# Performance work log

Measured on AMD Instinct MI355X. Metric: run time of the kernel, lower is better.

## Reference

```python
import jax, jax.numpy as jnp
import numpy as np

B, S, D = 2, 1024, 7168
H, HD, RD, QL = 64, 128, 64, 1536
EPS = 1e-6
SOFTMAX_SCALE = HD ** (-0.5)


def _rope_interleave(x, cos, sin):
    """Interleaved RoPE (pairs x[2i], x[2i+1]); x: [T, n, RD], cos/sin: [T, RD]."""
    x1 = x[..., 0::2]
    x2 = x[..., 1::2]
    c = cos[:, None, 0::2]
    s = sin[:, None, 0::2]
    o1 = x1 * c - x2 * s
    o2 = x2 * c + x1 * s
    return jnp.stack([o1, o2], axis=-1).reshape(x.shape)


def setup_inputs() -> dict:
    key = jax.random.key(0)
    ks = jax.random.split(key, 8)
    x = jax.random.normal(ks[0], (B, S, D), dtype=jnp.float32) * 0.02
    qr = jax.random.normal(ks[1], (B * S, QL), dtype=jnp.float32) * 0.02
    # real interleaved-RoPE cos/sin tables, tiled over batch
    pos = jnp.arange(S, dtype=jnp.float32)
    inv_freq = 1.0 / (10000.0 ** (jnp.arange(0, RD, 2, dtype=jnp.float32) / RD))
    freqs = pos[:, None] * inv_freq[None, :]                      # [S, RD/2]
    cos = jnp.repeat(jnp.cos(freqs), 2, axis=-1)                  # [S, RD]
    sin = jnp.repeat(jnp.sin(freqs), 2, axis=-1)
    cos = jnp.tile(cos, (B, 1))                                   # [B*S, RD]
    sin = jnp.tile(sin, (B, 1))
    wq_b_w = jax.random.normal(ks[2], (QL, H * HD), dtype=jnp.float32) * (QL ** -0.5)
    wk_w = jax.random.normal(ks[3], (D, HD), dtype=jnp.float32) * (D ** -0.5)
    wproj_w = jax.random.normal(ks[4], (D, H), dtype=jnp.float32) * (D ** -0.5)
    ln_gamma = jnp.ones((HD,), dtype=jnp.float32)
    ln_beta = jnp.ones((HD,), dtype=jnp.float32)  # module inits bias to ones
    return {"x": x, "qr": qr, "cos": cos, "sin": sin, "wq_b_w": wq_b_w,
            "wk_w": wk_w, "wproj_w": wproj_w, "ln_gamma": ln_gamma, "ln_beta": ln_beta}


def reference(x, qr, cos, sin, wq_b_w, wk_w, wproj_w, ln_gamma, ln_beta):
    b, s, d = x.shape
    t = b * s
    xf = x.reshape(t, d)
    # ---- query path: low-rank up-proj, split rope/nope, interleaved RoPE ----
    q = (qr @ wq_b_w).reshape(t, H, HD)
    q_pe, q_nope = q[..., :RD], q[..., RD:]
    q_pe = _rope_interleave(q_pe, cos, sin)
    q = jnp.concatenate([q_pe, q_nope], axis=-1).reshape(b, s, H, HD)
    # ---- per-head gating weights ----
    w = (xf @ wproj_w).reshape(b, s, H)
    # ---- key path: project, LayerNorm, RoPE on rope slice ----
    kp = xf @ wk_w                                                # [T, HD]
    mu = jnp.mean(kp, axis=-1, keepdims=True)
    var = jnp.mean(jnp.square(kp - mu), axis=-1, keepdims=True)
    kn = (kp - mu) * jax.lax.rsqrt(var + EPS) * ln_gamma + ln_beta
    k_pe, k_nope = kn[..., :RD], kn[..., RD:]
    k_pe = _rope_interleave(k_pe[:, None, :], cos, sin)[:, 0]
    k = jnp.concatenate([k_pe, k_nope], axis=-1).reshape(b, s, HD)
    # ---- lightning-indexer scores: weighted ReLU(q.k) summed over heads ----
    logits = jnp.einsum("bqhd,bkd->bqhk", q, k)                   # [B,S,H,S]
    scores = SOFTMAX_SCALE * jnp.einsum("bqh,bqhk->bqk", w, jax.nn.relu(logits))
    return scores
```

## Files before the change

### kernel.cpp

```cpp
#include <hip/hip_runtime.h>

typedef unsigned short u16;
typedef unsigned int   u32;

typedef __bf16 bf16x8 __attribute__((ext_vector_type(8)));
typedef float  f32x4  __attribute__((ext_vector_type(4)));

__device__ __forceinline__ float bf2f(u16 u){ u32 x = ((u32)u) << 16; return __builtin_bit_cast(float, x); }
__device__ __forceinline__ u16 f2bf(float f){
  u32 u = __builtin_bit_cast(u32, f);
  u32 r = (u + 0x7FFFu + ((u >> 16) & 1u)) >> 16;
  return (u16)r;
}
__device__ __forceinline__ u32 pk2bf(float a, float b){
  u32 ua = __builtin_bit_cast(u32, a) + 0x8000u;
  u32 ub = __builtin_bit_cast(u32, b) + 0x8000u;
  return __builtin_amdgcn_perm(ub, ua, 0x07060302u);
}
__device__ __forceinline__ void glds16(const void* g, void* l){
  __builtin_amdgcn_global_load_lds((const __attribute__((address_space(1))) void*)g,
                                   (__attribute__((address_space(3))) void*)l, 16, 0, 0);
}

__global__ __launch_bounds__(256) void transpose_f32_bf16(const float* __restrict__ src,
                                                          u16* __restrict__ dst, int R, int C){
  __shared__ u16 tile[32][33];
  int c0 = blockIdx.x * 32, r0 = blockIdx.y * 32;
  int tx = threadIdx.x & 31, ty = threadIdx.x >> 5;
  #pragma unroll
  for (int i = ty; i < 32; i += 8) tile[i][tx] = f2bf(src[(size_t)(r0 + i) * C + (c0 + tx)]);
  __syncthreads();
  #pragma unroll
  for (int i = ty; i < 32; i += 8) dst[(size_t)(c0 + i) * R + (r0 + tx)] = tile[tx][i];
}

__global__ __launch_bounds__(256) void cvt_f32_bf16(const float* __restrict__ src,
                                                    u16* __restrict__ dst){
  size_t i = ((size_t)blockIdx.x * 256 + threadIdx.x) * 8;
  const float4* a4 = (const float4*)(src + i);
  float4 f0 = a4[0], f1 = a4[1];
  u32 w[4] = { pk2bf(f0.x, f0.y), pk2bf(f0.z, f0.w), pk2bf(f1.x, f1.y), pk2bf(f1.z, f1.w) };
  *(uint4*)(dst + i) = *(const uint4*)w;
}

__global__ __launch_bounds__(256) void proj_splitk(const float* __restrict__ X,
    const u16* __restrict__ BT, float* __restrict__ P){
  constexpr int Kf = 7168;
  const int s = blockIdx.x, m0 = blockIdx.y * 64;
  const int kbase = s * 448;
  __shared__ u16 As[2 * 64 * 36];
  __shared__ u16 Bs[2 * 192 * 32];
  const int tid = threadIdx.x, wave = tid >> 6, lane = tid & 63;
  const int row = lane & 15, quad = lane >> 4;
  const int wm = (wave & 1) * 32, wn = (wave >> 1) * 96;

  const f32x4 zero = {0.f, 0.f, 0.f, 0.f};
  f32x4 acc[2][6];
  #pragma unroll
  for (int mt = 0; mt < 2; ++mt)
    #pragma unroll
    for (int nt = 0; nt < 6; ++nt) acc[mt][nt] = zero;

  for (int kb = 0; kb < 7; ++kb) {
    int k0 = kbase + kb * 64;
    #pragma unroll
    for (int c = 0; c < 6; ++c) {
      int chunk = wave * 6 + c;
      int kc = chunk / 12, rem = chunk % 12;
      int r = rem * 16 + (lane >> 2), col = (lane & 3) * 8;
      glds16(BT + (size_t)r * Kf + k0 + kc * 32 + col, (void*)&Bs[chunk * 512]);
    }
    #pragma unroll
    for (int c = 0; c < 2; ++c) {
      int idx = tid + c * 256;
      int r = idx >> 3, kf = (idx & 7) * 8;
      const float4* ap = (const float4*)(X + (size_t)(m0 + r) * Kf + k0 + kf);
      float4 f0 = ap[0], f1 = ap[1];
      u32 w[4] = { pk2bf(f0.x, f0.y), pk2bf(f0.z, f0.w), pk2bf(f1.x, f1.y), pk2bf(f1.z, f1.w) };
      *(uint4*)&As[(kf >> 5) * 2304 + r * 36 + (kf & 31)] = *(const uint4*)w;
    }
    __syncthreads();
    #pragma unroll
    for (int ks = 0; ks < 2; ++ks) {
      bf16x8 af[2], bfr[6];
      #pragma unroll
      for (int mt = 0; mt < 2; ++mt) af[mt] = *(const bf16x8*)&As[ks * 2304 + (wm + mt * 16 + row) * 36 + quad * 8];
      #pragma unroll
      for (int nt = 0; nt < 6; ++nt) bfr[nt] = *(const bf16x8*)&Bs[ks * 6144 + (wn + nt * 16 + row) * 32 + quad * 8];
      #pragma unroll
      for (int mt = 0; mt < 2; ++mt)
        #pragma unroll
        for (int nt = 0; nt < 6; ++nt)
          acc[mt][nt] = __builtin_amdgcn_mfma_f32_16x16x32_bf16(af[mt], bfr[nt], acc[mt][nt], 0, 0, 0);
    }
    __syncthreads();
  }
  #pragma unroll
  for (int mt = 0; mt < 2; ++mt)
    #pragma unroll
    for (int nt = 0; nt < 6; ++nt)
      #pragma unroll
      for (int r = 0; r < 4; ++r) {
        int rr = m0 + wm + mt * 16 + quad * 4 + r;
        int cc = wn + nt * 16 + row;
        P[((size_t)s * 2048 + rr) * 192 + cc] = acc[mt][nt][r];
      }
}

__global__ __launch_bounds__(64) void reduce_lnrope(const float* __restrict__ P,
    const float* __restrict__ cosb, const float* __restrict__ sinb,
    const float* __restrict__ gam, const float* __restrict__ bet,
    u16* __restrict__ Kout, float* __restrict__ WoutT){
  int tok = blockIdx.x, lane = threadIdx.x;
  float v0 = 0.f, v1 = 0.f, w = 0.f;
  #pragma unroll
  for (int s = 0; s < 16; ++s) {
    const float* p = P + ((size_t)s * 2048 + tok) * 192;
    v0 += p[2 * lane]; v1 += p[2 * lane + 1]; w += p[128 + lane];
  }
  WoutT[(size_t)lane * 2048 + tok] = w;
  float sm = v0 + v1;
  #pragma unroll
  for (int m = 1; m < 64; m <<= 1) sm += __shfl_xor(sm, m);
  float mu = sm * (1.f / 128.f);
  float d0 = v0 - mu, d1 = v1 - mu;
  float sq = d0 * d0 + d1 * d1;
  #pragma unroll
  for (int m = 1; m < 64; m <<= 1) sq += __shfl_xor(sq, m);
  float rs = rsqrtf(sq * (1.f / 128.f) + 1e-6f);
  float kn0 = d0 * rs * gam[2 * lane]     + bet[2 * lane];
  float kn1 = d1 * rs * gam[2 * lane + 1] + bet[2 * lane + 1];
  float o0 = kn0, o1 = kn1;
  if (lane < 32) {
    float c  = cosb[tok * 64 + 2 * lane];
    float sn = sinb[tok * 64 + 2 * lane];
    o0 = kn0 * c - kn1 * sn;
    o1 = kn1 * c + kn0 * sn;
  }
  Kout[tok * 128 + 2 * lane]     = f2bf(o0);
  Kout[tok * 128 + 2 * lane + 1] = f2bf(o1);
}

template<bool AGLDS>
__global__ __launch_bounds__(256) void qgemm(const void* __restrict__ Aptr,
    const u16* __restrict__ BT, const float* __restrict__ cosb,
    const float* __restrict__ sinb, u16* __restrict__ Qout){
  constexpr int K = 1536, N = 8192;
  __shared__ u16 As[2 * 128 * 32];
  __shared__ u16 Bs[2 * 128 * 32];
  const int tid = threadIdx.x, wave = tid >> 6, lane = tid & 63;
  const int row = lane & 15, quad = lane >> 4;
  const int wm = (wave >> 1) * 64, wn = (wave & 1) * 64;
  const int m0 = blockIdx.y * 128, n0 = blockIdx.x * 128;

  const f32x4 zero = {0.f, 0.f, 0.f, 0.f};
  f32x4 acc[4][4];
  #pragma unroll
  for (int mt = 0; mt < 4; ++mt)
    #pragma unroll
    for (int nt = 0; nt < 4; ++nt) acc[mt][nt] = zero;

  for (int k0 = 0; k0 < K; k0 += 64) {
    #pragma unroll
    for (int c = 0; c < 4; ++c) {
      int chunk = wave * 4 + c;
      int kc = chunk >> 3, rg = chunk & 7;
      int r = rg * 16 + (lane >> 2), col = kc * 32 + (lane & 3) * 8;
      glds16(BT + (size_t)(n0 + r) * K + k0 + col, (void*)&Bs[chunk * 512]);
    }
    if (AGLDS) {
      #pragma unroll
      for (int c = 0; c < 4; ++c) {
        int chunk = wave * 4 + c;
        int kc = chunk >> 3, rg = chunk & 7;
        int r = rg * 16 + (lane >> 2), col = kc * 32 + (lane & 3) * 8;
        glds16((const u16*)Aptr + (size_t)(m0 + r) * K + k0 + col, (void*)&As[chunk * 512]);
      }
    } else {
      #pragma unroll
      for (int c = 0; c < 4; ++c) {
        int idx = tid + c * 256;
        int r = idx >> 3, kf = (idx & 7) * 8;
        const float4* ap = (const float4*)((const float*)Aptr + (size_t)(m0 + r) * K + k0 + kf);
        float4 f0 = ap[0], f1 = ap[1];
        u32 w[4] = { pk2bf(f0.x, f0.y), pk2bf(f0.z, f0.w), pk2bf(f1.x, f1.y), pk2bf(f1.z, f1.w) };
        *(uint4*)&As[(kf >> 5) * 4096 + r * 32 + (kf & 31)] = *(const uint4*)w;
      }
    }
    __syncthreads();
    #pragma unroll
    for (int kk = 0; kk < 2; ++kk) {
      bf16x8 af[4], bfr[4];
      #pragma unroll
      for (int mt = 0; mt < 4; ++mt) af[mt]  = *(const bf16x8*)&As[kk * 4096 + (wm + mt * 16 + row) * 32 + quad * 8];
      #pragma unroll
      for (int nt = 0; nt < 4; ++nt) bfr[nt] = *(const bf16x8*)&Bs[kk * 4096 + (wn + nt * 16 + row) * 32 + quad * 8];
      #pragma unroll
      for (int mt = 0; mt < 4; ++mt)
        #pragma unroll
        for (int nt = 0; nt < 4; ++nt)
          acc[mt][nt] = __builtin_amdgcn_mfma_f32_16x16x32_bf16(af[mt], bfr[nt], acc[mt][nt], 0, 0, 0);
    }
    __syncthreads();
  }

  const bool roped = (wn == 0);
  #pragma unroll
  for (int mt = 0; mt < 4; ++mt)
    #pragma unroll
    for (int nt = 0; nt < 4; ++nt)
      #pragma unroll
      for (int r = 0; r < 4; ++r) {
        int rr = m0 + wm + mt * 16 + quad * 4 + r;
        int cc = n0 + wn + nt * 16 + row;
        float v = acc[mt][nt][r];
        float o = v;
        if (roped) {
          int hd = (wn + nt * 16 + row) & 127;
          float c = cosb[rr * 64 + hd];
          float s = sinb[rr * 64 + hd];
          float vo = __shfl_xor(v, 1);
          o = (cc & 1) ? (v * c + vo * s) : (v * c - vo * s);
        }
        Qout[(size_t)rr * N + cc] = f2bf(o);
      }
}

__global__ __launch_bounds__(256) void attn_kernel(const u16* __restrict__ Q,
    const u16* __restrict__ Kb, const float* __restrict__ WT, float* __restrict__ out){
  int blk = blockIdx.x;
  int x = blk & 7, kt = (blk >> 3) & 7, hs = (blk >> 6) & 1, g4 = (blk >> 7) & 3;
  int p = x + 8 * g4;
  int b = p >> 4, qt = p & 15;
  int q0 = qt * 64, k0 = kt * 128;

  const int tid = threadIdx.x, wave = tid >> 6, lane = tid & 63;
  const int row = lane & 15, quad = lane >> 4;
  const int wm = (wave >> 1) * 32;
  const int wn = (wave & 1) * 64;

  __shared__ u16 Sh[2 * 64 * 128];
  __shared__ float Ws[32 * 64];

  #pragma unroll
  for (int c = 0; c < 8; ++c) {
    int g = wave * 8 + c;
    int rr = g * 4 + (lane >> 4), col = (lane & 15) * 8;
    glds16(Kb + (size_t)(b * 1024 + k0 + rr) * 128 + col, (void*)&Sh[g * 512]);
  }
  {
    int hl = tid >> 3, qq = (tid & 7) * 8;
    const float* src = WT + (size_t)(hs * 32 + hl) * 2048 + b * 1024 + q0 + qq;
    *(float4*)&Ws[hl * 64 + qq]     = *(const float4*)src;
    *(float4*)&Ws[hl * 64 + qq + 4] = *(const float4*)(src + 4);
  }
  __syncthreads();

  bf16x8 bfr[4][4];
  #pragma unroll
  for (int ks = 0; ks < 4; ++ks)
    #pragma unroll
    for (int nt = 0; nt < 4; ++nt)
      bfr[ks][nt] = *(const bf16x8*)&Sh[(wn + nt * 16 + row) * 128 + ks * 32 + quad * 8];

  const f32x4 zero = {0.f, 0.f, 0.f, 0.f};
  f32x4 sacc[2][4];
  #pragma unroll
  for (int mt = 0; mt < 2; ++mt)
    #pragma unroll
    for (int nt = 0; nt < 4; ++nt) sacc[mt][nt] = zero;

  for (int hp = 0; hp < 16; ++hp) {
    int h0 = hs * 32 + hp * 2;
    __syncthreads();
    #pragma unroll
    for (int c = 0; c < 8; ++c) {
      int g = wave * 8 + c;
      int hsub = g >> 4, rem = g & 15;
      int kc = rem >> 2, rg = rem & 3;
      glds16(Q + (size_t)(b * 1024 + q0 + rg * 16 + (lane >> 2)) * 8192 + (h0 + hsub) * 128 + kc * 32 + (lane & 3) * 8,
             (void*)&Sh[hsub * 8192 + rem * 512]);
    }
    __syncthreads();

    #pragma unroll
    for (int hsub = 0; hsub < 2; ++hsub) {
      f32x4 lg[2][4];
      #pragma unroll
      for (int mt = 0; mt < 2; ++mt)
        #pragma unroll
        for (int nt = 0; nt < 4; ++nt) lg[mt][nt] = zero;
      #pragma unroll
      for (int ks = 0; ks < 4; ++ks) {
        bf16x8 af0 = *(const bf16x8*)&Sh[hsub * 8192 + ks * 2048 + (wm +      row) * 32 + quad * 8];
        bf16x8 af1 = *(const bf16x8*)&Sh[hsub * 8192 + ks * 2048 + (wm + 16 + row) * 32 + quad * 8];
        #pragma unroll
        for (int nt = 0; nt < 4; ++nt) {
          lg[0][nt] = __builtin_amdgcn_mfma_f32_16x16x32_bf16(af0, bfr[ks][nt], lg[0][nt], 0, 0, 0);
          lg[1][nt] = __builtin_amdgcn_mfma_f32_16x16x32_bf16(af1, bfr[ks][nt], lg[1][nt], 0, 0, 0);
        }
      }
      int hl = hp * 2 + hsub;
      f32x4 w0 = *(const f32x4*)&Ws[hl * 64 + wm +      quad * 4];
      f32x4 w1 = *(const f32x4*)&Ws[hl * 64 + wm + 16 + quad * 4];
      #pragma unroll
      for (int nt = 0; nt < 4; ++nt)
        #pragma unroll
        for (int r = 0; r < 4; ++r) {
          sacc[0][nt][r] += w0[r] * fmaxf(lg[0][nt][r], 0.f);
          sacc[1][nt][r] += w1[r] * fmaxf(lg[1][nt][r], 0.f);
        }
    }
  }

  const float scale = 0.088388347648318447f;
  #pragma unroll
  for (int mt = 0; mt < 2; ++mt)
    #pragma unroll
    for (int nt = 0; nt < 4; ++nt)
      #pragma unroll
      for (int r = 0; r < 4; ++r) {
        int qq = q0 + wm + mt * 16 + quad * 4 + r;
        int kk = k0 + wn + nt * 16 + row;
        unsafeAtomicAdd(&out[((size_t)b << 20) + (size_t)qq * 1024 + kk], scale * sacc[mt][nt][r]);
      }
}

extern "C" void kernel_launch(void* const* d_in, const int* in_sizes, int n_in,
                              void* d_out, int out_size, void* d_ws, size_t ws_size,
                              hipStream_t stream) {
  const float* x    = (const float*)d_in[0];
  const float* qr   = (const float*)d_in[1];
  const float* cosb = (const float*)d_in[2];
  const float* sinb = (const float*)d_in[3];
  const float* wq   = (const float*)d_in[4];
  const float* wk   = (const float*)d_in[5];
  const float* wp   = (const float*)d_in[6];
  const float* gam  = (const float*)d_in[7];
  const float* bet  = (const float*)d_in[8];
  float* out = (float*)d_out;

  char* ws = (char*)d_ws;
  float* P    = (float*)(ws + 0);
  u16*   wqT  = (u16*)(ws + 0);
  u16*   wkwpT= (u16*)(ws + 25165824);
  float* WT   = (float*)(ws + 27918336);
  u16*   Kbf  = (u16*)(ws + 28442624);
  u16*   Qbf  = (u16*)(ws + 28966912);
  const size_t QRB_OFF = 62521344;
  u16*   qrb  = (u16*)(ws + QRB_OFF);
  const bool big_ws = (ws_size >= (size_t)68812800);

  (void)in_sizes; (void)n_in;

  hipMemsetAsync(d_out, 0, (size_t)out_size * 4, stream);

  transpose_f32_bf16<<<dim3(4, 224),  256, 0, stream>>>(wk, wkwpT,              7168, 128);
  transpose_f32_bf16<<<dim3(2, 224),  256, 0, stream>>>(wp, wkwpT + 128 * 7168, 7168, 64);

  proj_splitk<<<dim3(16, 32), 256, 0, stream>>>(x, wkwpT, P);
  reduce_lnrope<<<2048, 64, 0, stream>>>(P, cosb, sinb, gam, bet, Kbf, WT);

  transpose_f32_bf16<<<dim3(256, 48), 256, 0, stream>>>(wq, wqT, 1536, 8192);

  if (big_ws) {
    cvt_f32_bf16<<<1536, 256, 0, stream>>>(qr, qrb);
    qgemm<true><<<dim3(64, 16), 256, 0, stream>>>(qrb, wqT, cosb, sinb, Qbf);
  } else {
    qgemm<false><<<dim3(64, 16), 256, 0, stream>>>(qr, wqT, cosb, sinb, Qbf);
  }

  attn_kernel<<<512, 256, 0, stream>>>(Qbf, Kbf, WT, out);
}
```

Before: 333.8 us.

## Vectorize weight transpose and double-buffer Q tiles in attention kernel

The fp32-to-bf16 transpose kernel now uses 64x64 tiles with float4 loads and 16-byte uint4 stores instead of scalar element accesses, cutting memory instruction count on the large wq transpose. The attention kernel splits shared memory into two Q buffers and prefetches the next head pair's Q tile with async global-to-LDS loads while the current pair is computed, removing one barrier per iteration. This doubles the attention kernel's shared memory footprint, which may lower occupancy. The transposed scatter into LDS uses a padded stride of 72, which may still cause some bank conflicts.

```diff
diff --git a/kernel.cpp b/kernel.cpp
--- a/kernel.cpp
+++ b/kernel.cpp
@@ -22,16 +22,30 @@
                                    (__attribute__((address_space(3))) void*)l, 16, 0, 0);
 }
 
-__global__ __launch_bounds__(256) void transpose_f32_bf16(const float* __restrict__ src,
-                                                          u16* __restrict__ dst, int R, int C){
-  __shared__ u16 tile[32][33];
-  int c0 = blockIdx.x * 32, r0 = blockIdx.y * 32;
-  int tx = threadIdx.x & 31, ty = threadIdx.x >> 5;
-  #pragma unroll
-  for (int i = ty; i < 32; i += 8) tile[i][tx] = f2bf(src[(size_t)(r0 + i) * C + (c0 + tx)]);
+__global__ __launch_bounds__(256) void transpose_f32_bf16_v(const float* __restrict__ src,
+                                                            u16* __restrict__ dst, int R, int C){
+  __shared__ u16 T[64 * 72];
+  int c0 = blockIdx.x * 64, r0 = blockIdx.y * 64;
+  int tr  = threadIdx.x >> 3;
+  int tc8 = (threadIdx.x & 7) * 8;
+  #pragma unroll
+  for (int it = 0; it < 2; ++it){
+    int rr = tr + it * 32;
+    const float* sp = src + (size_t)(r0 + rr) * C + c0 + tc8;
+    float4 f0 = *(const float4*)sp, f1 = *(const float4*)(sp + 4);
+    u16 v[8] = { f2bf(f0.x), f2bf(f0.y), f2bf(f0.z), f2bf(f0.w),
+                 f2bf(f1.x), f2bf(f1.y), f2bf(f1.z), f2bf(f1.w) };
+    #pragma unroll
+    for (int j = 0; j < 8; ++j) T[(tc8 + j) * 72 + rr] = v[j];
+  }
   __syncthreads();
-  #pragma unroll
-  for (int i = ty; i < 32; i += 8) dst[(size_t)(c0 + i) * R + (r0 + tx)] = tile[tx][i];
+  int tcw = threadIdx.x >> 3;
+  int tr8 = (threadIdx.x & 7) * 8;
+  #pragma unroll
+  for (int it = 0; it < 2; ++it){
+    int cc = tcw + it * 32;
+    *(uint4*)(dst + (size_t)(c0 + cc) * R + r0 + tr8) = *(const uint4*)&T[cc * 72 + tr8];
+  }
 }
 
 __global__ __launch_bounds__(256) void cvt_f32_bf16(const float* __restrict__ src,
@@ -239,20 +253,20 @@
   const int wm = (wave >> 1) * 32;
   const int wn = (wave & 1) * 64;
 
-  __shared__ u16 Sh[2 * 64 * 128];
+  __shared__ u16 Sh[2][16384];
   __shared__ float Ws[32 * 64];
 
   #pragma unroll
   for (int c = 0; c < 8; ++c) {
     int g = wave * 8 + c;
     int rr = g * 4 + (lane >> 4), col = (lane & 15) * 8;
-    glds16(Kb + (size_t)(b * 1024 + k0 + rr) * 128 + col, (void*)&Sh[g * 512]);
+    glds16(Kb + (size_t)(b * 1024 + k0 + rr) * 128 + col, (void*)&Sh[0][g * 512]);
   }
   {
     int hl = tid >> 3, qq = (tid & 7) * 8;
-    const float* src = WT + (size_t)(hs * 32 + hl) * 2048 + b * 1024 + q0 + qq;
-    *(float4*)&Ws[hl * 64 + qq]     = *(const float4*)src;
-    *(float4*)&Ws[hl * 64 + qq + 4] = *(const float4*)(src + 4);
+    const float* srcw = WT + (size_t)(hs * 32 + hl) * 2048 + b * 1024 + q0 + qq;
+    *(float4*)&Ws[hl * 64 + qq]     = *(const float4*)srcw;
+    *(float4*)&Ws[hl * 64 + qq + 4] = *(const float4*)(srcw + 4);
   }
   __syncthreads();
 
@@ -261,28 +275,34 @@
   for (int ks = 0; ks < 4; ++ks)
     #pragma unroll
     for (int nt = 0; nt < 4; ++nt)
-      bfr[ks][nt] = *(const bf16x8*)&Sh[(wn + nt * 16 + row) * 128 + ks * 32 + quad * 8];
-
-  const f32x4 zero = {0.f, 0.f, 0.f, 0.f};
-  f32x4 sacc[2][4];
-  #pragma unroll
-  for (int mt = 0; mt < 2; ++mt)
-    #pragma unroll
-    for (int nt = 0; nt < 4; ++nt) sacc[mt][nt] = zero;
-
-  for (int hp = 0; hp < 16; ++hp) {
-    int h0 = hs * 32 + hp * 2;
-    __syncthreads();
+      bfr[ks][nt] = *(const bf16x8*)&Sh[0][(wn + nt * 16 + row) * 128 + ks * 32 + quad * 8];
+  __syncthreads();
+
+  const u16* Qbase = Q + (size_t)(b * 1024 + q0) * 8192;
+  auto stage = [&](int half, int pairIdx){
+    int h0 = hs * 32 + pairIdx * 2;
     #pragma unroll
     for (int c = 0; c < 8; ++c) {
       int g = wave * 8 + c;
       int hsub = g >> 4, rem = g & 15;
       int kc = rem >> 2, rg = rem & 3;
-      glds16(Q + (size_t)(b * 1024 + q0 + rg * 16 + (lane >> 2)) * 8192 + (h0 + hsub) * 128 + kc * 32 + (lane & 3) * 8,
-             (void*)&Sh[hsub * 8192 + rem * 512]);
-    }
-    __syncthreads();
-
+      glds16(Qbase + (size_t)(rg * 16 + (lane >> 2)) * 8192 + (h0 + hsub) * 128 + kc * 32 + (lane & 3) * 8,
+             (void*)&Sh[half][hsub * 8192 + rem * 512]);
+    }
+  };
+
+  const f32x4 zero = {0.f, 0.f, 0.f, 0.f};
+  f32x4 sacc[2][4];
+  #pragma unroll
+  for (int mt = 0; mt < 2; ++mt)
+    #pragma unroll
+    for (int nt = 0; nt < 4; ++nt) sacc[mt][nt] = zero;
+
+  stage(0, 0);
+  for (int hp = 0; hp < 16; ++hp) {
+    __syncthreads();
+    if (hp < 15) stage((hp + 1) & 1, hp + 1);
+    const u16* S = Sh[hp & 1];
     #pragma unroll
     for (int hsub = 0; hsub < 2; ++hsub) {
       f32x4 lg[2][4];
@@ -292,8 +312,8 @@
         for (int nt = 0; nt < 4; ++nt) lg[mt][nt] = zero;
       #pragma unroll
       for (int ks = 0; ks < 4; ++ks) {
-        bf16x8 af0 = *(const bf16x8*)&Sh[hsub * 8192 + ks * 2048 + (wm +      row) * 32 + quad * 8];
-        bf16x8 af1 = *(const bf16x8*)&Sh[hsub * 8192 + ks * 2048 + (wm + 16 + row) * 32 + quad * 8];
+        bf16x8 af0 = *(const bf16x8*)&S[hsub * 8192 + ks * 2048 + (wm +      row) * 32 + quad * 8];
+        bf16x8 af1 = *(const bf16x8*)&S[hsub * 8192 + ks * 2048 + (wm + 16 + row) * 32 + quad * 8];
         #pragma unroll
         for (int nt = 0; nt < 4; ++nt) {
           lg[0][nt] = __builtin_amdgcn_mfma_f32_16x16x32_bf16(af0, bfr[ks][nt], lg[0][nt], 0, 0, 0);
@@ -355,13 +375,13 @@
 
   hipMemsetAsync(d_out, 0, (size_t)out_size * 4, stream);
 
-  transpose_f32_bf16<<<dim3(4, 224),  256, 0, stream>>>(wk, wkwpT,              7168, 128);
-  transpose_f32_bf16<<<dim3(2, 224),  256, 0, stream>>>(wp, wkwpT + 128 * 7168, 7168, 64);
+  transpose_f32_bf16_v<<<dim3(2, 112), 256, 0, stream>>>(wk, wkwpT,              7168, 128);
+  transpose_f32_bf16_v<<<dim3(1, 112), 256, 0, stream>>>(wp, wkwpT + 128 * 7168, 7168, 64);
 
   proj_splitk<<<dim3(16, 32), 256, 0, stream>>>(x, wkwpT, P);
   reduce_lnrope<<<2048, 64, 0, stream>>>(P, cosb, sinb, gam, bet, Kbf, WT);
 
-  transpose_f32_bf16<<<dim3(256, 48), 256, 0, stream>>>(wq, wqT, 1536, 8192);
+  transpose_f32_bf16_v<<<dim3(128, 24), 256, 0, stream>>>(wq, wqT, 1536, 8192);
 
   if (big_ws) {
     cvt_f32_bf16<<<1536, 256, 0, stream>>>(qr, qrb);
```

Measured after the change: 328.3 us. No clear change (-1.7%).
